# Performance work log

Hardware: AMD Instinct MI355X
Metric: run time of the kernel (lower is better)

Reference implementation:

```python
import jax, jax.numpy as jnp
import numpy as np

EPSILON = 0.5
B, N0, N1, N_DIM = 128, 128, 128, 32


def setup_inputs() -> dict:
    key = jax.random.key(0)
    ks = jax.random.split(key, 7)
    X = jax.random.normal(ks[0], (B, N_DIM), dtype=jnp.float32)
    t = jax.random.uniform(ks[1], (1,), dtype=jnp.float32, minval=0.05, maxval=0.95)
    Mu0 = jax.random.normal(ks[2], (N0, N_DIM), dtype=jnp.float32)
    Mu1 = jax.random.normal(ks[3], (N1, N_DIM), dtype=jnp.float32)
    # positive diagonal variances
    S0 = jax.random.uniform(ks[4], (N0, N_DIM), dtype=jnp.float32) + 0.5
    S1 = jax.random.uniform(ks[5], (N1, N_DIM), dtype=jnp.float32) + 0.5
    # nonnegative coupling that sums to 1 (stand-in for the EMD plan)
    Lam = jax.random.uniform(ks[6], (N0, N1), dtype=jnp.float32)
    Lam = Lam / jnp.sum(Lam)
    return {"X": X, "t": t, "Mu0": Mu0, "Mu1": Mu1, "S0": S0, "S1": S1, "Lam": Lam}


def reference(X, t, Mu0, Mu1, S0, S1, Lam):
    """GMMflow.calc_u: Gaussian-mixture weighted drift u(X, t)."""
    eps = EPSILON
    t = t.reshape(())  # scalar time
    S0b = S0[:, None, :]   # [N0, 1, n]
    S1b = S1[None, :, :]   # [1, N1, n]
    Ds = jnp.sqrt(4.0 * S0b * S1b + eps ** 4)          # [N0, N1, n]
    Cs = 0.5 * (Ds - eps ** 2)
    Sigma = ((1 - t) ** 2) * S0b + (t ** 2) * S1b + 2 * t * (1 - t) * Cs + (eps ** 2) * t * (1 - t)
    Pt = t * S1b + (1 - t) * Cs
    Qt = (1 - t) * S0b + t * Cs
    St = Pt - Qt - (eps ** 2) * t
    Mut = (1 - t) * Mu0[:, None, :] + t * Mu1[None, :, :]   # [N0, N1, n]
    v = Mu1[None, :, :] - Mu0[:, None, :]                   # [N0, N1, n]
    K = St / Sigma                                          # [N0, N1, n]

    D = X[:, None, None, :] - Mut[None]                     # [B, N0, N1, n]
    U = K[None] * D + v[None]                               # [B, N0, N1, n]
    # Independent-Normal log_prob with the +n/2*log(2*pi) offset cancelled
    logw = jnp.sum(-0.5 * D * D / Sigma[None] - 0.5 * jnp.log(Sigma)[None], axis=-1)  # [B, N0, N1]
    W = jnp.exp(jnp.clip(logw, -50.0, 50.0)) * Lam[None]    # [B, N0, N1]

    num = jnp.einsum('bijn,bij->bn', U, W)                  # weighted drift sum
    den = jnp.sum(W, axis=(1, 2))                           # [B]
    return num / den[:, None]
```

## Files before the change

kernel.cpp:

```cpp
#include <hip/hip_runtime.h>
#include <math.h>

#define BB 128
#define ND 32
#define NIJ 16384
#define EPS2 0.25f
#define EPS4 0.0625f

#define TIJ 64
#define NBLK (NIJ / TIJ)
#define NTHR 1024
#define ROWF 132

#define XS_OFF  8448
#define CC_OFF  13056
#define LAM_OFF 13120
#define LDS_FL  13184
#define STG_ROW 36

#define PART_STRIDE 4224
#define DEN_OFF_P 4096

__global__ __launch_bounds__(NTHR, 4) void gmm_fused(
    const float* __restrict__ Xg,
    const float* __restrict__ tptr,
    const float* __restrict__ Mu0, const float* __restrict__ Mu1,
    const float* __restrict__ S0,  const float* __restrict__ S1,
    const float* __restrict__ Lam,
    float* __restrict__ part)
{
    __shared__ __align__(16) float lds[LDS_FL];

    const int tid  = threadIdx.x;
    const int blk  = blockIdx.x;
    const int ij0g = blk * TIJ;
    const float t   = tptr[0];
    const float omt = 1.0f - t;

    {
        const int r  = tid >> 3;
        const int c4 = (tid & 7) * 4;
        *(float4*)&lds[XS_OFF + r * STG_ROW + c4] =
            *(const float4*)&Xg[tid * 4];
    }

#pragma unroll
    for (int k = 0; k < (TIJ * ND) / NTHR; ++k) {
        const int idx = tid + k * NTHR;
        const int ijl = idx >> 5;
        const int n   = idx & 31;
        const int ij  = ij0g + ijl;
        const int i   = ij >> 7;
        const int j   = ij & 127;
        const float s0  = S0[i * ND + n];
        const float s1  = S1[j * ND + n];
        const float mu0 = Mu0[i * ND + n];
        const float mu1 = Mu1[j * ND + n];
        const float Ds  = sqrtf(4.0f * s0 * s1 + EPS4);
        const float Cs  = 0.5f * (Ds - EPS2);
        const float Sigma = omt * omt * s0 + t * t * s1
                          + 2.0f * t * omt * Cs + EPS2 * t * omt;
        const float St  = (t * s1 + omt * Cs) - (omt * s0 + t * Cs) - EPS2 * t;
        const float Mut = omt * mu0 + t * mu1;
        const float v   = mu1 - mu0;
        const float invS = 1.0f / Sigma;
        const float Kf  = St * invS;
        const float cA  = -0.5f * invS;
        const float cB  = Mut * invS;
        lds[ijl * ROWF + n]      = cA;
        lds[ijl * ROWF + 32 + n] = cB;
        lds[ijl * ROWF + 64 + n] = Kf;
        lds[ijl * ROWF + 96 + n] = v - Kf * Mut;
        float cc = cA * Mut * Mut - 0.5f * __logf(Sigma);
        cc += __shfl_xor(cc, 1);
        cc += __shfl_xor(cc, 2);
        cc += __shfl_xor(cc, 4);
        cc += __shfl_xor(cc, 8);
        cc += __shfl_xor(cc, 16);
        if (n == 0) lds[CC_OFF + ijl] = cc;
    }
    if (tid < TIJ) lds[LAM_OFF + tid] = Lam[ij0g + tid];

    __syncthreads();

    const int gij = tid & 7;
    const int nh  = (tid >> 3) & 1;
    const int bl  = tid >> 4;
    const int n0  = nh * 16;

    float x0[16], x1[16];
#pragma unroll
    for (int c = 0; c < 4; ++c) {
        const float4 v4 = *(const float4*)&lds[XS_OFF + bl * STG_ROW + n0 + 4 * c];
        const float4 w4 = *(const float4*)&lds[XS_OFF + (bl + 64) * STG_ROW + n0 + 4 * c];
        x0[4*c+0] = v4.x; x0[4*c+1] = v4.y; x0[4*c+2] = v4.z; x0[4*c+3] = v4.w;
        x1[4*c+0] = w4.x; x1[4*c+1] = w4.y; x1[4*c+2] = w4.z; x1[4*c+3] = w4.w;
    }

    float num0[16], num1[16];
#pragma unroll
    for (int n = 0; n < 16; ++n) { num0[n] = 0.0f; num1[n] = 0.0f; }
    float den0 = 0.0f, den1 = 0.0f;

#pragma unroll 2
    for (int it = 0; it < TIJ / 8; ++it) {
        const int ijl = gij + (it << 3);
        const float* __restrict__ row = &lds[ijl * ROWF + n0];
        float la0 = 0.0f, lb0 = 0.0f;
        float la1 = 0.0f, lb1 = 0.0f;
#pragma unroll
        for (int nc = 0; nc < 4; ++nc) {
            const float4 a  = *(const float4*)&row[nc * 4];
            const float4 bq = *(const float4*)&row[32 + nc * 4];
            la0 = fmaf(fmaf(a.x, x0[nc*4+0], bq.x), x0[nc*4+0], la0);
            lb0 = fmaf(fmaf(a.y, x0[nc*4+1], bq.y), x0[nc*4+1], lb0);
            la0 = fmaf(fmaf(a.z, x0[nc*4+2], bq.z), x0[nc*4+2], la0);
            lb0 = fmaf(fmaf(a.w, x0[nc*4+3], bq.w), x0[nc*4+3], lb0);
            la1 = fmaf(fmaf(a.x, x1[nc*4+0], bq.x), x1[nc*4+0], la1);
            lb1 = fmaf(fmaf(a.y, x1[nc*4+1], bq.y), x1[nc*4+1], lb1);
            la1 = fmaf(fmaf(a.z, x1[nc*4+2], bq.z), x1[nc*4+2], la1);
            lb1 = fmaf(fmaf(a.w, x1[nc*4+3], bq.w), x1[nc*4+3], lb1);
        }
        float lw0 = la0 + lb0;  lw0 += __shfl_xor(lw0, 8);
        float lw1 = la1 + lb1;  lw1 += __shfl_xor(lw1, 8);
        const float cc0 = lds[CC_OFF + ijl];
        const float lam = lds[LAM_OFF + ijl];
        lw0 = fminf(fmaxf(lw0 + cc0, -50.0f), 50.0f);
        lw1 = fminf(fmaxf(lw1 + cc0, -50.0f), 50.0f);
        const float w0 = __expf(lw0) * lam;
        const float w1 = __expf(lw1) * lam;
        den0 += w0; den1 += w1;
#pragma unroll
        for (int nc = 0; nc < 4; ++nc) {
            const float4 kk = *(const float4*)&row[64 + nc * 4];
            const float4 kv = *(const float4*)&row[96 + nc * 4];
            num0[nc*4+0] = fmaf(w0, fmaf(kk.x, x0[nc*4+0], kv.x), num0[nc*4+0]);
            num0[nc*4+1] = fmaf(w0, fmaf(kk.y, x0[nc*4+1], kv.y), num0[nc*4+1]);
            num0[nc*4+2] = fmaf(w0, fmaf(kk.z, x0[nc*4+2], kv.z), num0[nc*4+2]);
            num0[nc*4+3] = fmaf(w0, fmaf(kk.w, x0[nc*4+3], kv.w), num0[nc*4+3]);
            num1[nc*4+0] = fmaf(w1, fmaf(kk.x, x1[nc*4+0], kv.x), num1[nc*4+0]);
            num1[nc*4+1] = fmaf(w1, fmaf(kk.y, x1[nc*4+1], kv.y), num1[nc*4+1]);
            num1[nc*4+2] = fmaf(w1, fmaf(kk.z, x1[nc*4+2], kv.z), num1[nc*4+2]);
            num1[nc*4+3] = fmaf(w1, fmaf(kk.w, x1[nc*4+3], kv.w), num1[nc*4+3]);
        }
    }

#pragma unroll
    for (int c = 0; c < 8; ++c) {
        const float s0v = (gij & 4) ? num0[c] : num0[c + 8];
        const float s1v = (gij & 4) ? num1[c] : num1[c + 8];
        const float r0 = __shfl_xor(s0v, 4);
        const float r1 = __shfl_xor(s1v, 4);
        num0[c] = ((gij & 4) ? num0[c + 8] : num0[c]) + r0;
        num1[c] = ((gij & 4) ? num1[c + 8] : num1[c]) + r1;
    }
#pragma unroll
    for (int c = 0; c < 4; ++c) {
        const float s0v = (gij & 2) ? num0[c] : num0[c + 4];
        const float s1v = (gij & 2) ? num1[c] : num1[c + 4];
        const float r0 = __shfl_xor(s0v, 2);
        const float r1 = __shfl_xor(s1v, 2);
        num0[c] = ((gij & 2) ? num0[c + 4] : num0[c]) + r0;
        num1[c] = ((gij & 2) ? num1[c + 4] : num1[c]) + r1;
    }
#pragma unroll
    for (int c = 0; c < 2; ++c) {
        const float s0v = (gij & 1) ? num0[c] : num0[c + 2];
        const float s1v = (gij & 1) ? num1[c] : num1[c + 2];
        const float r0 = __shfl_xor(s0v, 1);
        const float r1 = __shfl_xor(s1v, 1);
        num0[c] = ((gij & 1) ? num0[c + 2] : num0[c]) + r0;
        num1[c] = ((gij & 1) ? num1[c + 2] : num1[c]) + r1;
    }

    den0 += __shfl_xor(den0, 1);
    den0 += __shfl_xor(den0, 2);
    den0 += __shfl_xor(den0, 4);
    den1 += __shfl_xor(den1, 1);
    den1 += __shfl_xor(den1, 2);
    den1 += __shfl_xor(den1, 4);

    float* __restrict__ dstg = part + (size_t)blk * PART_STRIDE;
    *(float2*)(dstg + bl * 32 + n0 + 2 * gij) =
        make_float2(num0[0], num0[1]);
    *(float2*)(dstg + (bl + 64) * 32 + n0 + 2 * gij) =
        make_float2(num1[0], num1[1]);
    if ((tid & 15) == 0) {
        dstg[DEN_OFF_P + bl]      = den0;
        dstg[DEN_OFF_P + bl + 64] = den1;
    }
}

__global__ __launch_bounds__(256) void gmm_reduce(
    const float* __restrict__ part,
    float* __restrict__ out)
{
    const int blk = blockIdx.x;
    const int b   = blk >> 1;
    const int nh  = blk & 1;
    const int tid = threadIdx.x;
    const int n16 = tid & 15;
    const int sg  = tid >> 4;
    const int n   = nh * 16 + n16;

    float num = 0.0f, den = 0.0f;
#pragma unroll
    for (int g = 0; g < 16; ++g) {
        const int s = sg + g * 16;
        const size_t base = (size_t)s * PART_STRIDE;
        num += part[base + b * 32 + n];
        den += part[base + DEN_OFF_P + b];
    }

    __shared__ float red[16][18];
    red[sg][n16] = num;
    if (n16 == 0) red[sg][16] = den;
    __syncthreads();

    if (tid < 16) {
        float ns = 0.0f, ds = 0.0f;
#pragma unroll
        for (int k = 0; k < 16; ++k) {
            ns += red[k][tid];
            ds += red[k][16];
        }
        out[b * 32 + nh * 16 + tid] = ns / ds;
    }
}

extern "C" void kernel_launch(void* const* d_in, const int* in_sizes, int n_in,
                              void* d_out, int out_size, void* d_ws, size_t ws_size,
                              hipStream_t stream)
{
    const float* X   = (const float*)d_in[0];
    const float* t   = (const float*)d_in[1];
    const float* Mu0 = (const float*)d_in[2];
    const float* Mu1 = (const float*)d_in[3];
    const float* S0  = (const float*)d_in[4];
    const float* S1  = (const float*)d_in[5];
    const float* Lam = (const float*)d_in[6];
    float* out  = (float*)d_out;
    float* part = (float*)d_ws;

    gmm_fused<<<NBLK, NTHR, 0, stream>>>(X, t, Mu0, Mu1, S0, S1, Lam, part);
    gmm_reduce<<<2 * BB, 256, 0, stream>>>(part, out);
}
```

Measured before the change: 81.37 us.

## Register-block four batch rows by eight dims per thread in fused kernel

Changes the thread mapping in the main loop: each thread now handles 4 batch rows over 8 feature dims, instead of 2 rows over 16 dims. Each coefficient vector loaded from LDS is then reused across four rows, which cuts shared-memory read traffic per FMA. The price is an extra cross-lane shuffle for the log-weight reduction and a fully unrolled inner loop. Register pressure also rises, which could reduce occupancy or cause spills under the launch bounds.

```diff
diff --git a/kernel.cpp b/kernel.cpp
--- a/kernel.cpp
+++ b/kernel.cpp
@@ -84,110 +84,115 @@
     __syncthreads();
 
     const int gij = tid & 7;
-    const int nh  = (tid >> 3) & 1;
-    const int bl  = tid >> 4;
-    const int n0  = nh * 16;
-
-    float x0[16], x1[16];
-#pragma unroll
-    for (int c = 0; c < 4; ++c) {
-        const float4 v4 = *(const float4*)&lds[XS_OFF + bl * STG_ROW + n0 + 4 * c];
-        const float4 w4 = *(const float4*)&lds[XS_OFF + (bl + 64) * STG_ROW + n0 + 4 * c];
-        x0[4*c+0] = v4.x; x0[4*c+1] = v4.y; x0[4*c+2] = v4.z; x0[4*c+3] = v4.w;
-        x1[4*c+0] = w4.x; x1[4*c+1] = w4.y; x1[4*c+2] = w4.z; x1[4*c+3] = w4.w;
-    }
-
-    float num0[16], num1[16];
-#pragma unroll
-    for (int n = 0; n < 16; ++n) { num0[n] = 0.0f; num1[n] = 0.0f; }
-    float den0 = 0.0f, den1 = 0.0f;
-
-#pragma unroll 2
+    const int nq  = (tid >> 3) & 3;
+    const int bl  = tid >> 5;
+    const int n0  = nq * 8;
+
+    float x[4][8];
+#pragma unroll
+    for (int rb = 0; rb < 4; ++rb) {
+        const float4 v4 = *(const float4*)&lds[XS_OFF + (bl + 32 * rb) * STG_ROW + n0];
+        const float4 w4 = *(const float4*)&lds[XS_OFF + (bl + 32 * rb) * STG_ROW + n0 + 4];
+        x[rb][0] = v4.x; x[rb][1] = v4.y; x[rb][2] = v4.z; x[rb][3] = v4.w;
+        x[rb][4] = w4.x; x[rb][5] = w4.y; x[rb][6] = w4.z; x[rb][7] = w4.w;
+    }
+
+    float num[4][8];
+#pragma unroll
+    for (int rb = 0; rb < 4; ++rb)
+#pragma unroll
+        for (int n = 0; n < 8; ++n) num[rb][n] = 0.0f;
+    float den[4] = {0.0f, 0.0f, 0.0f, 0.0f};
+
+#pragma unroll
     for (int it = 0; it < TIJ / 8; ++it) {
         const int ijl = gij + (it << 3);
         const float* __restrict__ row = &lds[ijl * ROWF + n0];
-        float la0 = 0.0f, lb0 = 0.0f;
-        float la1 = 0.0f, lb1 = 0.0f;
-#pragma unroll
-        for (int nc = 0; nc < 4; ++nc) {
-            const float4 a  = *(const float4*)&row[nc * 4];
-            const float4 bq = *(const float4*)&row[32 + nc * 4];
-            la0 = fmaf(fmaf(a.x, x0[nc*4+0], bq.x), x0[nc*4+0], la0);
-            lb0 = fmaf(fmaf(a.y, x0[nc*4+1], bq.y), x0[nc*4+1], lb0);
-            la0 = fmaf(fmaf(a.z, x0[nc*4+2], bq.z), x0[nc*4+2], la0);
-            lb0 = fmaf(fmaf(a.w, x0[nc*4+3], bq.w), x0[nc*4+3], lb0);
-            la1 = fmaf(fmaf(a.x, x1[nc*4+0], bq.x), x1[nc*4+0], la1);
-            lb1 = fmaf(fmaf(a.y, x1[nc*4+1], bq.y), x1[nc*4+1], lb1);
-            la1 = fmaf(fmaf(a.z, x1[nc*4+2], bq.z), x1[nc*4+2], la1);
-            lb1 = fmaf(fmaf(a.w, x1[nc*4+3], bq.w), x1[nc*4+3], lb1);
-        }
-        float lw0 = la0 + lb0;  lw0 += __shfl_xor(lw0, 8);
-        float lw1 = la1 + lb1;  lw1 += __shfl_xor(lw1, 8);
+        const float4 a0 = *(const float4*)&row[0];
+        const float4 a1 = *(const float4*)&row[4];
+        const float4 b0 = *(const float4*)&row[32];
+        const float4 b1 = *(const float4*)&row[36];
+
+        float la[4], lb[4];
+#pragma unroll
+        for (int rb = 0; rb < 4; ++rb) {
+            float u = fmaf(fmaf(a0.x, x[rb][0], b0.x), x[rb][0], 0.0f);
+            float v = fmaf(fmaf(a0.y, x[rb][1], b0.y), x[rb][1], 0.0f);
+            u = fmaf(fmaf(a0.z, x[rb][2], b0.z), x[rb][2], u);
+            v = fmaf(fmaf(a0.w, x[rb][3], b0.w), x[rb][3], v);
+            u = fmaf(fmaf(a1.x, x[rb][4], b1.x), x[rb][4], u);
+            v = fmaf(fmaf(a1.y, x[rb][5], b1.y), x[rb][5], v);
+            u = fmaf(fmaf(a1.z, x[rb][6], b1.z), x[rb][6], u);
+            v = fmaf(fmaf(a1.w, x[rb][7], b1.w), x[rb][7], v);
+            la[rb] = u; lb[rb] = v;
+        }
+
+        const float4 k0 = *(const float4*)&row[64];
+        const float4 k1 = *(const float4*)&row[68];
+        const float4 v0 = *(const float4*)&row[96];
+        const float4 v1 = *(const float4*)&row[100];
         const float cc0 = lds[CC_OFF + ijl];
         const float lam = lds[LAM_OFF + ijl];
-        lw0 = fminf(fmaxf(lw0 + cc0, -50.0f), 50.0f);
-        lw1 = fminf(fmaxf(lw1 + cc0, -50.0f), 50.0f);
-        const float w0 = __expf(lw0) * lam;
-        const float w1 = __expf(lw1) * lam;
-        den0 += w0; den1 += w1;
-#pragma unroll
-        for (int nc = 0; nc < 4; ++nc) {
-            const float4 kk = *(const float4*)&row[64 + nc * 4];
-            const float4 kv = *(const float4*)&row[96 + nc * 4];
-            num0[nc*4+0] = fmaf(w0, fmaf(kk.x, x0[nc*4+0], kv.x), num0[nc*4+0]);
-            num0[nc*4+1] = fmaf(w0, fmaf(kk.y, x0[nc*4+1], kv.y), num0[nc*4+1]);
-            num0[nc*4+2] = fmaf(w0, fmaf(kk.z, x0[nc*4+2], kv.z), num0[nc*4+2]);
-            num0[nc*4+3] = fmaf(w0, fmaf(kk.w, x0[nc*4+3], kv.w), num0[nc*4+3]);
-            num1[nc*4+0] = fmaf(w1, fmaf(kk.x, x1[nc*4+0], kv.x), num1[nc*4+0]);
-            num1[nc*4+1] = fmaf(w1, fmaf(kk.y, x1[nc*4+1], kv.y), num1[nc*4+1]);
-            num1[nc*4+2] = fmaf(w1, fmaf(kk.z, x1[nc*4+2], kv.z), num1[nc*4+2]);
-            num1[nc*4+3] = fmaf(w1, fmaf(kk.w, x1[nc*4+3], kv.w), num1[nc*4+3]);
-        }
-    }
-
-#pragma unroll
-    for (int c = 0; c < 8; ++c) {
-        const float s0v = (gij & 4) ? num0[c] : num0[c + 8];
-        const float s1v = (gij & 4) ? num1[c] : num1[c + 8];
-        const float r0 = __shfl_xor(s0v, 4);
-        const float r1 = __shfl_xor(s1v, 4);
-        num0[c] = ((gij & 4) ? num0[c + 8] : num0[c]) + r0;
-        num1[c] = ((gij & 4) ? num1[c + 8] : num1[c]) + r1;
-    }
-#pragma unroll
-    for (int c = 0; c < 4; ++c) {
-        const float s0v = (gij & 2) ? num0[c] : num0[c + 4];
-        const float s1v = (gij & 2) ? num1[c] : num1[c + 4];
-        const float r0 = __shfl_xor(s0v, 2);
-        const float r1 = __shfl_xor(s1v, 2);
-        num0[c] = ((gij & 2) ? num0[c + 4] : num0[c]) + r0;
-        num1[c] = ((gij & 2) ? num1[c + 4] : num1[c]) + r1;
-    }
-#pragma unroll
-    for (int c = 0; c < 2; ++c) {
-        const float s0v = (gij & 1) ? num0[c] : num0[c + 2];
-        const float s1v = (gij & 1) ? num1[c] : num1[c + 2];
-        const float r0 = __shfl_xor(s0v, 1);
-        const float r1 = __shfl_xor(s1v, 1);
-        num0[c] = ((gij & 1) ? num0[c + 2] : num0[c]) + r0;
-        num1[c] = ((gij & 1) ? num1[c + 2] : num1[c]) + r1;
-    }
-
-    den0 += __shfl_xor(den0, 1);
-    den0 += __shfl_xor(den0, 2);
-    den0 += __shfl_xor(den0, 4);
-    den1 += __shfl_xor(den1, 1);
-    den1 += __shfl_xor(den1, 2);
-    den1 += __shfl_xor(den1, 4);
+
+        float w[4];
+#pragma unroll
+        for (int rb = 0; rb < 4; ++rb) {
+            float lw = la[rb] + lb[rb];
+            lw += __shfl_xor(lw, 8);
+            lw += __shfl_xor(lw, 16);
+            lw = fminf(fmaxf(lw + cc0, -50.0f), 50.0f);
+            w[rb] = __expf(lw) * lam;
+            den[rb] += w[rb];
+        }
+
+#pragma unroll
+        for (int rb = 0; rb < 4; ++rb) {
+            num[rb][0] = fmaf(w[rb], fmaf(k0.x, x[rb][0], v0.x), num[rb][0]);
+            num[rb][1] = fmaf(w[rb], fmaf(k0.y, x[rb][1], v0.y), num[rb][1]);
+            num[rb][2] = fmaf(w[rb], fmaf(k0.z, x[rb][2], v0.z), num[rb][2]);
+            num[rb][3] = fmaf(w[rb], fmaf(k0.w, x[rb][3], v0.w), num[rb][3]);
+            num[rb][4] = fmaf(w[rb], fmaf(k1.x, x[rb][4], v1.x), num[rb][4]);
+            num[rb][5] = fmaf(w[rb], fmaf(k1.y, x[rb][5], v1.y), num[rb][5]);
+            num[rb][6] = fmaf(w[rb], fmaf(k1.z, x[rb][6], v1.z), num[rb][6]);
+            num[rb][7] = fmaf(w[rb], fmaf(k1.w, x[rb][7], v1.w), num[rb][7]);
+        }
+    }
+
+#pragma unroll
+    for (int rb = 0; rb < 4; ++rb) {
+#pragma unroll
+        for (int c = 0; c < 4; ++c) {
+            const float s = (gij & 4) ? num[rb][c] : num[rb][c + 4];
+            const float r = __shfl_xor(s, 4);
+            num[rb][c] = ((gij & 4) ? num[rb][c + 4] : num[rb][c]) + r;
+        }
+#pragma unroll
+        for (int c = 0; c < 2; ++c) {
+            const float s = (gij & 2) ? num[rb][c] : num[rb][c + 2];
+            const float r = __shfl_xor(s, 2);
+            num[rb][c] = ((gij & 2) ? num[rb][c + 2] : num[rb][c]) + r;
+        }
+        {
+            const float s = (gij & 1) ? num[rb][0] : num[rb][1];
+            const float r = __shfl_xor(s, 1);
+            num[rb][0] = ((gij & 1) ? num[rb][1] : num[rb][0]) + r;
+        }
+        den[rb] += __shfl_xor(den[rb], 1);
+        den[rb] += __shfl_xor(den[rb], 2);
+        den[rb] += __shfl_xor(den[rb], 4);
+    }
 
     float* __restrict__ dstg = part + (size_t)blk * PART_STRIDE;
-    *(float2*)(dstg + bl * 32 + n0 + 2 * gij) =
-        make_float2(num0[0], num0[1]);
-    *(float2*)(dstg + (bl + 64) * 32 + n0 + 2 * gij) =
-        make_float2(num1[0], num1[1]);
-    if ((tid & 15) == 0) {
-        dstg[DEN_OFF_P + bl]      = den0;
-        dstg[DEN_OFF_P + bl + 64] = den1;
+    const int col = (tid & 31);
+#pragma unroll
+    for (int rb = 0; rb < 4; ++rb) {
+        dstg[(bl + 32 * rb) * 32 + col] = num[rb][0];
+    }
+    if (col == 0) {
+#pragma unroll
+        for (int rb = 0; rb < 4; ++rb) {
+            dstg[DEN_OFF_P + bl + 32 * rb] = den[rb];
+        }
     }
 }
 
```

New measurement: 82.04 us. No clear change (+0.8%).
